# Performance work log

Hardware: AMD Instinct MI355X
Metric: run time of the kernel (lower is better)

## Reference

```python
import jax, jax.numpy as jnp
import numpy as np

DIM = 1024
NUM_HEADS = 16
HEAD_DIM = DIM // NUM_HEADS
SCALE = HEAD_DIM ** -0.5


def setup_inputs() -> dict:
    key = jax.random.key(0)
    ks = jax.random.split(key, 12)
    B, N, M, C = 4, 512, 2048, DIM
    x = jax.random.normal(ks[0], (B, N, C), dtype=jnp.float32)
    context = jax.random.normal(ks[1], (B, M, C), dtype=jnp.float32)
    mask = jax.random.randint(ks[2], (B, M), 0, 2, dtype=jnp.int32)
    mask = mask.at[:, 0].set(1)  # ensure at least one valid key per row
    w = 0.02
    Wq = jax.random.normal(ks[3], (C, C), dtype=jnp.float32) * w
    bq = jnp.zeros((C,), dtype=jnp.float32)
    Wk = jax.random.normal(ks[4], (C, C), dtype=jnp.float32) * w
    bk = jnp.zeros((C,), dtype=jnp.float32)
    Wv = jax.random.normal(ks[5], (C, C), dtype=jnp.float32) * w
    bv = jnp.zeros((C,), dtype=jnp.float32)
    Wo = jax.random.normal(ks[6], (C, C), dtype=jnp.float32) * w
    bo = jnp.zeros((C,), dtype=jnp.float32)
    return {"x": x, "context": context, "ctx_key_padding_mask": mask,
            "Wq": Wq, "bq": bq, "Wk": Wk, "bk": bk,
            "Wv": Wv, "bv": bv, "Wo": Wo, "bo": bo}


def reference(x, context, ctx_key_padding_mask, Wq, bq, Wk, bk, Wv, bv, Wo, bo):
    B, N, C = x.shape
    M = context.shape[1]
    H, D = NUM_HEADS, HEAD_DIM
    # torch nn.Linear: y = x @ W.T + b
    q = (x @ Wq.T + bq).reshape(B, N, H, D)
    k = (context @ Wk.T + bk).reshape(B, M, H, D)
    v = (context @ Wv.T + bv).reshape(B, M, H, D)
    scores = jnp.einsum('bnhd,bmhd->bhnm', q, k) * SCALE  # [B,H,N,M]
    neg = jnp.finfo(scores.dtype).min
    bias = jnp.where(ctx_key_padding_mask[:, None, None, :] != 0, 0.0, neg).astype(scores.dtype)
    attn = jax.nn.softmax(scores + bias, axis=-1)
    out = jnp.einsum('bhnm,bmhd->bnhd', attn, v).reshape(B, N, C)
    return out @ Wo.T + bo
```

## Files before the change

kernel.cpp:

```cpp
#include <hip/hip_runtime.h>
#include <hip/hip_bf16.h>
#include <stdint.h>


typedef __attribute__((ext_vector_type(4))) float f32x4;
typedef __attribute__((ext_vector_type(8))) __bf16 bf16x8;
typedef __attribute__((ext_vector_type(8))) unsigned short u16x8;

#define DEVI __device__ __forceinline__

#define QSC (0.125f * 1.44269504088896f)

DEVI f32x4 mfma16(u16x8 a, u16x8 b, f32x4 c) {
  return __builtin_amdgcn_mfma_f32_16x16x32_bf16(
      __builtin_bit_cast(bf16x8, a), __builtin_bit_cast(bf16x8, b), c, 0, 0, 0);
}

DEVI unsigned short f2bf(float f) {
  union { float f; unsigned int u; } x; x.f = f;
  unsigned int u = x.u;
  return (unsigned short)((u + 0x7fffu + ((u >> 16) & 1u)) >> 16);
}

DEVI float exp2_fast(float x) {
#if __has_builtin(__builtin_amdgcn_exp2f)
  return __builtin_amdgcn_exp2f(x);
#else
  return exp2f(x);
#endif
}

DEVI void llds16(const void* g, void* l) {
  __builtin_amdgcn_global_load_lds(
      (const __attribute__((address_space(1))) void*)g,
      (__attribute__((address_space(3))) void*)l, 16, 0, 0);
}

__global__ __launch_bounds__(256)
void mask_meta(const int* __restrict__ mask, int* __restrict__ meta,
               int* __restrict__ cnt) {
  const int b = blockIdx.x;
  const int tid = threadIdx.x;
  const int* mb = mask + b * 2048;
  int v[8], s = 0;
#pragma unroll
  for (int j = 0; j < 8; ++j) { v[j] = (mb[tid * 8 + j] != 0) ? 1 : 0; s += v[j]; }
  __shared__ int sc[2][256];
  sc[0][tid] = s;
  __syncthreads();
  int src = 0;
  for (int off = 1; off < 256; off <<= 1) {
    int x = sc[src][tid];
    if (tid >= off) x += sc[src][tid - off];
    sc[src ^ 1][tid] = x;
    src ^= 1;
    __syncthreads();
  }
  const int incl = sc[src][tid];
  const int c = sc[src][255];
  int pre = incl - s;
#pragma unroll
  for (int j = 0; j < 8; ++j) {
    const int p = tid * 8 + j;
    const unsigned dst = v[j] ? (unsigned)pre : (unsigned)(c + (p - pre));
    meta[b * 2048 + p] = (int)(dst | (v[j] ? 0x80000000u : 0u));
    pre += v[j];
  }
  if (tid == 0) cnt[b] = c;
}

__global__ __launch_bounds__(256)
void cast_fused(const float* __restrict__ x, const float* __restrict__ ctx,
                const float* __restrict__ wq, const float* __restrict__ wk,
                const float* __restrict__ wv, const float* __restrict__ wo,
                const int* __restrict__ meta, const int* __restrict__ cnt,
                unsigned short* __restrict__ xb, unsigned short* __restrict__ cb,
                unsigned short* __restrict__ wqb, unsigned short* __restrict__ wkb,
                unsigned short* __restrict__ wvb, unsigned short* __restrict__ wob) {
  int bid = blockIdx.x;
  const int tid = threadIdx.x;
  if (bid >= 512 && bid < 2560) {
    const int r0 = (bid - 512) * 4;
#pragma unroll
    for (int rr = 0; rr < 4; ++rr) {
      const int r = r0 + rr;
      const int b = r >> 11;
      const unsigned mv = (unsigned)meta[r];
      const int valid = (int)(mv >> 31);
      const int dst = (int)(mv & 0x7fffffffu);
      if (!valid && dst >= ((cnt[b] + 255) & ~255)) continue;
      unsigned short* dp = cb + ((size_t)(b * 2048 + dst)) * 1024 + tid * 4;
      if (valid) {
        const float4 v = *(const float4*)(ctx + ((size_t)r) * 1024 + tid * 4);
        ushort4 o;
        o.x = f2bf(v.x); o.y = f2bf(v.y); o.z = f2bf(v.z); o.w = f2bf(v.w);
        *(ushort4*)dp = o;
      } else {
        ushort4 z; z.x = z.y = z.z = z.w = 0;
        *(ushort4*)dp = z;
      }
    }
    return;
  }
  const float* src; unsigned short* dst; float scale = 1.f;
  if (bid < 512) { src = x; dst = xb; }
  else {
    bid -= 2560;
    const int w = bid >> 8; bid &= 255;
    src = (w == 0) ? wq : (w == 1) ? wk : (w == 2) ? wv : wo;
    dst = (w == 0) ? wqb : (w == 1) ? wkb : (w == 2) ? wvb : wob;
    if (w == 0) scale = QSC;
  }
  const int e0 = bid * 4096 + tid * 4;
#pragma unroll
  for (int it = 0; it < 4; ++it) {
    const int e = e0 + it * 1024;
    const float4 v = *(const float4*)(src + e);
    ushort4 o;
    o.x = f2bf(v.x * scale); o.y = f2bf(v.y * scale);
    o.z = f2bf(v.z * scale); o.w = f2bf(v.w * scale);
    *(ushort4*)(dst + e) = o;
  }
}

DEVI void epi_store(f32x4 (&acc)[4][4], const float* __restrict__ bias,
                    float bscale, void* __restrict__ Cout,
                    int bm, int bn, int logS, int mode,
                    unsigned short* cst, int tid, int wave, int l15, int quad) {
  const int wm = wave & 1, wn = wave >> 1;
  __syncthreads();
  for (int half = 0; half < 2; ++half) {
    if (wm == half) {
#pragma unroll
      for (int mi = 0; mi < 4; ++mi)
#pragma unroll
        for (int ni = 0; ni < 4; ++ni)
#pragma unroll
          for (int r = 0; r < 4; ++r) {
            int lrow = mi * 16 + quad * 4 + r;
            int lcol = wn * 64 + ni * 16 + l15;
            unsigned short bv = f2bf(acc[mi][ni][r] + bias[bn + lcol] * bscale);
            if (mode == 0) cst[lrow * 136 + lcol] = bv;
            else           cst[lcol * 72 + lrow] = bv;
          }
    }
    __syncthreads();
    if (mode == 0) {
      int lrow = tid >> 2, cc = (tid & 3) * 32;
      int row = bm + half * 64 + lrow;
      int S = 1 << logS;
      int b = row >> logS, sl = row & (S - 1);
#pragma unroll
      for (int j = 0; j < 4; ++j) {
        int col = bn + cc + j * 8;
        int h = col >> 6, d8 = (col & 63) >> 3;
        size_t base = (((size_t)(b * 16 + h)) << logS) * 64 +
                      (size_t)(sl >> 4) * 1024 + d8 * 128 + (sl & 15) * 8;
        *(u16x8*)&((unsigned short*)Cout)[base] =
            *(const u16x8*)&cst[lrow * 136 + cc + j * 8];
      }
    } else {
      int c = tid >> 1, rc = (tid & 1) * 32;
      int gc = bn + c, h = gc >> 6, d = gc & 63;
      int b = bm >> 11;
#pragma unroll
      for (int j = 0; j < 4; ++j) {
        int key = (bm & 2047) + half * 64 + rc + j * 8;
        size_t base = (size_t)(b * 16 + h) * 131072 +
                      (size_t)(((key >> 6) * 4 + (d >> 4)) * 8 + ((key >> 3) & 7)) * 128 +
                      (d & 15) * 8;
        *(u16x8*)&((unsigned short*)Cout)[base] =
            *(const u16x8*)&cst[c * 72 + rc + j * 8];
      }
    }
    __syncthreads();
  }
}

DEVI void kv_body(const unsigned short* __restrict__ A,
                  const unsigned short* __restrict__ WK,
                  const unsigned short* __restrict__ WV,
                  const float* __restrict__ bk, const float* __restrict__ bv,
                  unsigned short* __restrict__ kh, unsigned short* __restrict__ vt,
                  int bm, int bn, unsigned short* sh) {
  constexpr int K = 1024;
  unsigned short* As = sh;
  unsigned short* Ks = sh + 128 * 64;
  unsigned short* Vs = sh + 2 * 128 * 64;

  const int tid = threadIdx.x;
  const int wave = tid >> 6, lane = tid & 63;
  const int l15 = lane & 15, quad = lane >> 4;
  const int wm = wave & 1, wn = wave >> 1;

  f32x4 ak[4][4] = {}, av[4][4] = {};

  for (int k0 = 0; k0 < K; k0 += 64) {
    __syncthreads();
#pragma unroll
    for (int c = 0; c < 4; ++c) {
      int s = c * 256 + tid;
      int m = s >> 3;
      int k8 = (s & 7) ^ (m & 7);
      llds16(A + (size_t)(bm + m) * K + k0 + k8 * 8, &As[s * 8]);
      llds16(WK + (size_t)(bn + m) * K + k0 + k8 * 8, &Ks[s * 8]);
      llds16(WV + (size_t)(bn + m) * K + k0 + k8 * 8, &Vs[s * 8]);
    }
    __syncthreads();
#pragma unroll
    for (int ks = 0; ks < 2; ++ks) {
      const int k8 = ks * 4 + quad;
      u16x8 af[4], bf[4];
#pragma unroll
      for (int i = 0; i < 4; ++i) {
        int m = wm * 64 + i * 16 + l15;
        af[i] = *(const u16x8*)(&As[(m * 8 + (k8 ^ (m & 7))) * 8]);
      }
#pragma unroll
      for (int i = 0; i < 4; ++i) {
        int n = wn * 64 + i * 16 + l15;
        bf[i] = *(const u16x8*)(&Ks[(n * 8 + (k8 ^ (n & 7))) * 8]);
      }
#pragma unroll
      for (int mi = 0; mi < 4; ++mi)
#pragma unroll
        for (int ni = 0; ni < 4; ++ni)
          ak[mi][ni] = mfma16(af[mi], bf[ni], ak[mi][ni]);
#pragma unroll
      for (int i = 0; i < 4; ++i) {
        int n = wn * 64 + i * 16 + l15;
        bf[i] = *(const u16x8*)(&Vs[(n * 8 + (k8 ^ (n & 7))) * 8]);
      }
#pragma unroll
      for (int mi = 0; mi < 4; ++mi)
#pragma unroll
        for (int ni = 0; ni < 4; ++ni)
          av[mi][ni] = mfma16(af[mi], bf[ni], av[mi][ni]);
    }
  }

  epi_store(ak, bk, 1.f, kh, bm, bn, 11, 0, sh, tid, wave, l15, quad);
  epi_store(av, bv, 1.f, vt, bm, bn, 11, 2, sh, tid, wave, l15, quad);
}

DEVI void q_body(const unsigned short* __restrict__ A,
                 const unsigned short* __restrict__ W,
                 const float* __restrict__ bias,
                 unsigned short* __restrict__ Cout,
                 int bm, int bn, unsigned short* sh) {
  constexpr int K = 1024;
  unsigned short* As = sh;
  unsigned short* Bs = sh + 128 * 64;

  const int tid = threadIdx.x;
  const int wave = tid >> 6, lane = tid & 63;
  const int l15 = lane & 15, quad = lane >> 4;
  const int wm = wave & 1, wn = wave >> 1;

  f32x4 acc[4][4] = {};

  for (int k0 = 0; k0 < K; k0 += 64) {
    __syncthreads();
#pragma unroll
    for (int c = 0; c < 4; ++c) {
      int s = c * 256 + tid;
      int m = s >> 3;
      int k8 = (s & 7) ^ (m & 7);
      llds16(A + (size_t)(bm + m) * K + k0 + k8 * 8, &As[s * 8]);
      llds16(W + (size_t)(bn + m) * K + k0 + k8 * 8, &Bs[s * 8]);
    }
    __syncthreads();
#pragma unroll
    for (int ks = 0; ks < 2; ++ks) {
      const int k8 = ks * 4 + quad;
      u16x8 af[4], bf[4];
#pragma unroll
      for (int i = 0; i < 4; ++i) {
        int m = wm * 64 + i * 16 + l15;
        af[i] = *(const u16x8*)(&As[(m * 8 + (k8 ^ (m & 7))) * 8]);
        int n = wn * 64 + i * 16 + l15;
        bf[i] = *(const u16x8*)(&Bs[(n * 8 + (k8 ^ (n & 7))) * 8]);
      }
#pragma unroll
      for (int mi = 0; mi < 4; ++mi)
#pragma unroll
        for (int ni = 0; ni < 4; ++ni)
          acc[mi][ni] = mfma16(af[mi], bf[ni], acc[mi][ni]);
    }
  }

  epi_store(acc, bias, QSC, Cout, bm, bn, 9, 0, sh, tid, wave, l15, quad);
}

__global__ __launch_bounds__(256, 2)
void gemm_qkv(const unsigned short* __restrict__ xb,
              const unsigned short* __restrict__ cb,
              const unsigned short* __restrict__ wq,
              const unsigned short* __restrict__ wk,
              const unsigned short* __restrict__ wv,
              const float* __restrict__ bq, const float* __restrict__ bk,
              const float* __restrict__ bv,
              const int* __restrict__ cnt,
              unsigned short* __restrict__ qh, unsigned short* __restrict__ kh,
              unsigned short* __restrict__ vt) {
  __shared__ __align__(16) unsigned short sh[128 * 64 * 3];
  const int id = blockIdx.x;

  const int nb0 = ((cnt[0] + 255) & ~255) >> 7;
  const int nb1 = ((cnt[1] + 255) & ~255) >> 7;
  const int nb2 = ((cnt[2] + 255) & ~255) >> 7;
  const int nb3 = ((cnt[3] + 255) & ~255) >> 7;
  const int L = nb0 + nb1 + nb2 + nb3;
  if (id < L * 8) {
    int xl = id >> 3, y = id & 7, b = 0;
    if (xl >= nb0) { xl -= nb0; b = 1;
      if (xl >= nb1) { xl -= nb1; b = 2;
        if (xl >= nb2) { xl -= nb2; b = 3; } } }
    kv_body(cb, wk, wv, bk, bv, kh, vt, b * 2048 + xl * 128, y * 128, sh);
  } else if (id < L * 8 + 128) {
    const int q = id - L * 8;
    q_body(xb, wq, bq, qh, (q & 15) * 128, (q >> 4) * 128, sh);
  }
}

__global__ __launch_bounds__(256)
void gemm_o(const unsigned short* __restrict__ A,
            const unsigned short* __restrict__ W,
            const float* __restrict__ bo, float* __restrict__ out) {
  constexpr int K = 1024;
  __shared__ __align__(16) unsigned short As[64 * 64];
  __shared__ __align__(16) unsigned short Bs[128 * 64];

  const int tid = threadIdx.x;
  const int wave = tid >> 6, lane = tid & 63;
  const int l15 = lane & 15, quad = lane >> 4;
  const int bm = blockIdx.x * 64, bn = blockIdx.y * 128;

  f32x4 acc[4][2] = {};

  for (int k0 = 0; k0 < K; k0 += 64) {
    __syncthreads();
#pragma unroll
    for (int c = 0; c < 2; ++c) {
      int s = c * 256 + tid;
      int m = s >> 3, k8 = (s & 7) ^ (m & 7);
      llds16(A + (size_t)(bm + m) * K + k0 + k8 * 8, &As[s * 8]);
    }
#pragma unroll
    for (int c = 0; c < 4; ++c) {
      int s = c * 256 + tid;
      int m = s >> 3, k8 = (s & 7) ^ (m & 7);
      llds16(W + (size_t)(bn + m) * K + k0 + k8 * 8, &Bs[s * 8]);
    }
    __syncthreads();
#pragma unroll
    for (int ks = 0; ks < 2; ++ks) {
      const int k8 = ks * 4 + quad;
      u16x8 af[4], bf[2];
#pragma unroll
      for (int i = 0; i < 4; ++i) {
        int m = i * 16 + l15;
        af[i] = *(const u16x8*)(&As[(m * 8 + (k8 ^ (m & 7))) * 8]);
      }
#pragma unroll
      for (int i = 0; i < 2; ++i) {
        int n = wave * 32 + i * 16 + l15;
        bf[i] = *(const u16x8*)(&Bs[(n * 8 + (k8 ^ (n & 7))) * 8]);
      }
#pragma unroll
      for (int mi = 0; mi < 4; ++mi)
#pragma unroll
        for (int ni = 0; ni < 2; ++ni)
          acc[mi][ni] = mfma16(af[mi], bf[ni], acc[mi][ni]);
    }
  }

#pragma unroll
  for (int mi = 0; mi < 4; ++mi)
#pragma unroll
    for (int ni = 0; ni < 2; ++ni)
#pragma unroll
      for (int r = 0; r < 4; ++r) {
        int row = bm + mi * 16 + quad * 4 + r;
        int col = bn + wave * 32 + ni * 16 + l15;
        out[(size_t)row * 1024 + col] = acc[mi][ni][r] + bo[col];
      }
}

#define PS 72
__global__ __launch_bounds__(256, 2)
void attn_kernel(const unsigned short* __restrict__ Q,
                 const unsigned short* __restrict__ K,
                 const unsigned short* __restrict__ Vt,
                 const int* __restrict__ cnt,
                 unsigned short* __restrict__ O) {
  __shared__ __align__(16) unsigned short p_lds[4][2][16 * PS];
  __shared__ float l_lds[4][64];
  __shared__ __align__(16) float o_comb[64][68];

  const int tid = threadIdx.x;
  const int wave = tid >> 6, lane = tid & 63;
  const int l15 = lane & 15, quad = lane >> 4;
  const int bh = blockIdx.x, b = bh >> 4, h = bh & 15;
  const int q0 = blockIdx.y * 64;

  const int c = cnt[b];
  const int T = (c + 255) >> 8;

  const unsigned short* Qb = Q + (size_t)bh * 32768 + (size_t)(q0 >> 4) * 1024;
  const unsigned short* Kb = K + (size_t)bh * 131072;
  const unsigned short* Vb = Vt + (size_t)bh * 131072;

  u16x8 aq[4][2];
#pragma unroll
  for (int qg = 0; qg < 4; ++qg)
#pragma unroll
    for (int ks = 0; ks < 2; ++ks)
      aq[qg][ks] = *(const u16x8*)(Qb + ((qg * 8 + ks * 4 + quad) * 16 + l15) * 8);

  f32x4 o_acc[4][4] = {};
  float l_s[4] = {0.f, 0.f, 0.f, 0.f};

  u16x8 kf[2][4];

  auto load_k = [&](int kb) {
    const int kg0 = kb >> 4;
#pragma unroll
    for (int ns = 0; ns < 4; ++ns)
#pragma unroll
      for (int ks = 0; ks < 2; ++ks)
        kf[ks][ns] = *(const u16x8*)(Kb + (((size_t)(kg0 + ns) * 8 + ks * 4 + quad) * 16 + l15) * 8);
  };

  load_k(wave * 64);

#pragma unroll 1
  for (int t = 0; t < T; ++t) {
    const int kb = wave * 64 + t * 256;
    const int kb_next = kb + (t + 1 < T ? 256 : 0);

    u16x8 vf[2][4];
    const int kt4 = (kb >> 6) * 4;
#pragma unroll
    for (int nd = 0; nd < 4; ++nd)
#pragma unroll
      for (int ks = 0; ks < 2; ++ks)
        vf[ks][nd] = *(const u16x8*)(Vb + (((size_t)(kt4 + nd) * 8 + ks * 4 + quad) * 16 + l15) * 8);

    f32x4 bfr[4];
    if (kb + 64 <= c) {
#pragma unroll
      for (int ns = 0; ns < 4; ++ns)
        bfr[ns] = f32x4{-8.f, -8.f, -8.f, -8.f};
    } else {
#pragma unroll
      for (int ns = 0; ns < 4; ++ns)
#pragma unroll
        for (int r = 0; r < 4; ++r)
          bfr[ns][r] = (kb + ns * 16 + quad * 4 + r < c) ? -8.f : -1e30f;
    }

#pragma unroll
    for (int qg = 0; qg < 4; ++qg) {
      f32x4 sfr[4];
#pragma unroll
      for (int ns = 0; ns < 4; ++ns) {
        f32x4 sa = bfr[ns];
#pragma unroll
        for (int ks = 0; ks < 2; ++ks)
          sa = mfma16(kf[ks][ns], aq[qg][ks], sa);
        sfr[ns] = sa;
      }

      if (qg == 3) load_k(kb_next);

      float rsum = 0.f;
#pragma unroll
      for (int ns = 0; ns < 4; ++ns) {
        unsigned int pr[4];
#pragma unroll
        for (int r = 0; r < 4; ++r) {
          float p = exp2_fast(sfr[ns][r]);
          unsigned int u = __builtin_bit_cast(unsigned int, p) & 0xffff0000u;
          rsum += __builtin_bit_cast(float, u);
          pr[r] = u;
        }
        uint2 pw;
        pw.x = __builtin_amdgcn_perm(pr[1], pr[0], 0x07060302u);
        pw.y = __builtin_amdgcn_perm(pr[3], pr[2], 0x07060302u);
        *(uint2*)&p_lds[wave][qg & 1][l15 * PS + ns * 16 + quad * 4] = pw;
      }
      rsum += __shfl_xor(rsum, 16, 64);
      rsum += __shfl_xor(rsum, 32, 64);
      l_s[qg] += rsum;

#pragma unroll
      for (int ks = 0; ks < 2; ++ks) {
        u16x8 pf = *(const u16x8*)&p_lds[wave][qg & 1][l15 * PS + ks * 32 + quad * 8];
#pragma unroll
        for (int nd = 0; nd < 4; ++nd)
          o_acc[qg][nd] = mfma16(pf, vf[ks][nd], o_acc[qg][nd]);
      }
    }
  }

  if (quad == 0) {
#pragma unroll
    for (int qg = 0; qg < 4; ++qg)
      l_lds[wave][qg * 16 + l15] = l_s[qg];
  }
  __syncthreads();

  for (int w = 0; w < 4; ++w) {
    if (wave == w) {
#pragma unroll
      for (int qg = 0; qg < 4; ++qg)
#pragma unroll
        for (int r = 0; r < 4; ++r) {
          const int q = qg * 16 + quad * 4 + r;
#pragma unroll
          for (int nd = 0; nd < 4; ++nd) {
            const int d = nd * 16 + l15;
            float v = o_acc[qg][nd][r];
            if (w == 0) o_comb[q][d] = v;
            else        o_comb[q][d] += v;
          }
        }
    }
    __syncthreads();
  }

  {
    const int q = tid >> 2, dc = (tid & 3) * 16;
    const float inv = 1.f / (l_lds[0][q] + l_lds[1][q] + l_lds[2][q] + l_lds[3][q]);
    unsigned short* Ob = O + ((size_t)(b * 512 + q0 + q)) * 1024 + h * 64 + dc;
    u16x8 o1, o2;
#pragma unroll
    for (int j = 0; j < 8; ++j) o1[j] = f2bf(o_comb[q][dc + j] * inv);
#pragma unroll
    for (int j = 0; j < 8; ++j) o2[j] = f2bf(o_comb[q][dc + 8 + j] * inv);
    *(u16x8*)(Ob) = o1;
    *(u16x8*)(Ob + 8) = o2;
  }
}

extern "C" void kernel_launch(void* const* d_in, const int* in_sizes, int n_in,
                              void* d_out, int out_size, void* d_ws, size_t ws_size,
                              hipStream_t stream) {
  const float* x   = (const float*)d_in[0];
  const float* ctx = (const float*)d_in[1];
  const int* mask  = (const int*)d_in[2];
  const float* Wq  = (const float*)d_in[3];
  const float* bq  = (const float*)d_in[4];
  const float* Wk  = (const float*)d_in[5];
  const float* bk  = (const float*)d_in[6];
  const float* Wv  = (const float*)d_in[7];
  const float* bv  = (const float*)d_in[8];
  const float* Wo  = (const float*)d_in[9];
  const float* bo  = (const float*)d_in[10];

  char* ws = (char*)d_ws;
  unsigned short* xb  = (unsigned short*)(ws + ((size_t)0  << 20));
  unsigned short* cb  = (unsigned short*)(ws + ((size_t)4  << 20));
  unsigned short* wqb = (unsigned short*)(ws + ((size_t)20 << 20));
  unsigned short* wkb = (unsigned short*)(ws + ((size_t)22 << 20));
  unsigned short* wvb = (unsigned short*)(ws + ((size_t)24 << 20));
  unsigned short* wob = (unsigned short*)(ws + ((size_t)26 << 20));
  unsigned short* qh  = (unsigned short*)(ws + ((size_t)28 << 20));
  unsigned short* kh  = (unsigned short*)(ws + ((size_t)32 << 20));
  unsigned short* vt  = (unsigned short*)(ws + ((size_t)48 << 20));
  unsigned short* ah  = (unsigned short*)(ws + ((size_t)64 << 20));
  int* meta           = (int*)(ws + ((size_t)68 << 20));
  int* cntp           = meta + 8192;

  mask_meta<<<4, 256, 0, stream>>>(mask, meta, cntp);
  cast_fused<<<3584, 256, 0, stream>>>(x, ctx, Wq, Wk, Wv, Wo, meta, cntp,
                                       xb, cb, wqb, wkb, wvb, wob);
  gemm_qkv<<<640, 256, 0, stream>>>(xb, cb, wqb, wkb, wvb,
                                    bq, bk, bv, cntp, qh, kh, vt);
  attn_kernel<<<dim3(64, 8), 256, 0, stream>>>(qh, kh, vt, cntp, ah);
  gemm_o<<<dim3(32, 8), 256, 0, stream>>>(ah, wob, bo, (float*)d_out);
}
```

Before: 187.0 us.

## Fuse context gather and bf16 cast into KV GEMM, merge mask scan into cast

Drops the separate pass that compacted and cast the fp32 context into a bf16 buffer. The KV GEMM now gathers fp32 context rows through a source-index table, converts them to bf16 in registers, and writes them into LDS itself. The mask prefix-scan moves into the cast kernel's first four blocks, which removes one launch. This saves a full read and write of the context intermediate. In exchange the GEMM's A-operand path goes from async global-to-LDS copies to synchronous fp32 register loads that move twice the bytes, and each KV tile over 8 column blocks redoes the fp32 reads and conversion.

After: 194.4 us. 1.04x slower.

```diff
diff --git a/kernel.cpp b/kernel.cpp
--- a/kernel.cpp
+++ b/kernel.cpp
@@ -6,6 +6,7 @@
 typedef __attribute__((ext_vector_type(4))) float f32x4;
 typedef __attribute__((ext_vector_type(8))) __bf16 bf16x8;
 typedef __attribute__((ext_vector_type(8))) unsigned short u16x8;
+typedef __attribute__((ext_vector_type(4))) unsigned int u32x4;
 
 #define DEVI __device__ __forceinline__
 
@@ -20,6 +21,14 @@
   union { float f; unsigned int u; } x; x.f = f;
   unsigned int u = x.u;
   return (unsigned short)((u + 0x7fffu + ((u >> 16) & 1u)) >> 16);
+}
+
+DEVI unsigned int pack2(float lo, float hi) {
+  unsigned int ul = __builtin_bit_cast(unsigned int, lo);
+  unsigned int uh = __builtin_bit_cast(unsigned int, hi);
+  ul += 0x7fffu + ((ul >> 16) & 1u);
+  uh += 0x7fffu + ((uh >> 16) & 1u);
+  return __builtin_amdgcn_perm(uh, ul, 0x07060302u);
 }
 
 DEVI float exp2_fast(float x) {
@@ -37,75 +46,51 @@
 }
 
 __global__ __launch_bounds__(256)
-void mask_meta(const int* __restrict__ mask, int* __restrict__ meta,
-               int* __restrict__ cnt) {
-  const int b = blockIdx.x;
-  const int tid = threadIdx.x;
-  const int* mb = mask + b * 2048;
-  int v[8], s = 0;
-#pragma unroll
-  for (int j = 0; j < 8; ++j) { v[j] = (mb[tid * 8 + j] != 0) ? 1 : 0; s += v[j]; }
-  __shared__ int sc[2][256];
-  sc[0][tid] = s;
-  __syncthreads();
-  int src = 0;
-  for (int off = 1; off < 256; off <<= 1) {
-    int x = sc[src][tid];
-    if (tid >= off) x += sc[src][tid - off];
-    sc[src ^ 1][tid] = x;
-    src ^= 1;
-    __syncthreads();
-  }
-  const int incl = sc[src][tid];
-  const int c = sc[src][255];
-  int pre = incl - s;
-#pragma unroll
-  for (int j = 0; j < 8; ++j) {
-    const int p = tid * 8 + j;
-    const unsigned dst = v[j] ? (unsigned)pre : (unsigned)(c + (p - pre));
-    meta[b * 2048 + p] = (int)(dst | (v[j] ? 0x80000000u : 0u));
-    pre += v[j];
-  }
-  if (tid == 0) cnt[b] = c;
-}
-
-__global__ __launch_bounds__(256)
-void cast_fused(const float* __restrict__ x, const float* __restrict__ ctx,
+void cast_fused(const float* __restrict__ x,
                 const float* __restrict__ wq, const float* __restrict__ wk,
                 const float* __restrict__ wv, const float* __restrict__ wo,
-                const int* __restrict__ meta, const int* __restrict__ cnt,
-                unsigned short* __restrict__ xb, unsigned short* __restrict__ cb,
+                const int* __restrict__ mask,
+                int* __restrict__ isrc, int* __restrict__ cnt,
+                unsigned short* __restrict__ xb,
                 unsigned short* __restrict__ wqb, unsigned short* __restrict__ wkb,
                 unsigned short* __restrict__ wvb, unsigned short* __restrict__ wob) {
   int bid = blockIdx.x;
   const int tid = threadIdx.x;
-  if (bid >= 512 && bid < 2560) {
-    const int r0 = (bid - 512) * 4;
-#pragma unroll
-    for (int rr = 0; rr < 4; ++rr) {
-      const int r = r0 + rr;
-      const int b = r >> 11;
-      const unsigned mv = (unsigned)meta[r];
-      const int valid = (int)(mv >> 31);
-      const int dst = (int)(mv & 0x7fffffffu);
-      if (!valid && dst >= ((cnt[b] + 255) & ~255)) continue;
-      unsigned short* dp = cb + ((size_t)(b * 2048 + dst)) * 1024 + tid * 4;
-      if (valid) {
-        const float4 v = *(const float4*)(ctx + ((size_t)r) * 1024 + tid * 4);
-        ushort4 o;
-        o.x = f2bf(v.x); o.y = f2bf(v.y); o.z = f2bf(v.z); o.w = f2bf(v.w);
-        *(ushort4*)dp = o;
-      } else {
-        ushort4 z; z.x = z.y = z.z = z.w = 0;
-        *(ushort4*)dp = z;
-      }
-    }
+  if (bid < 4) {
+    const int b = bid;
+    const int* mb = mask + b * 2048;
+    int v[8], s = 0;
+#pragma unroll
+    for (int j = 0; j < 8; ++j) { v[j] = (mb[tid * 8 + j] != 0) ? 1 : 0; s += v[j]; }
+    __shared__ int sc[2][256];
+    sc[0][tid] = s;
+    __syncthreads();
+    int src = 0;
+    for (int off = 1; off < 256; off <<= 1) {
+      int xv = sc[src][tid];
+      if (tid >= off) xv += sc[src][tid - off];
+      sc[src ^ 1][tid] = xv;
+      src ^= 1;
+      __syncthreads();
+    }
+    const int incl = sc[src][tid];
+    const int c = sc[src][255];
+    int pre = incl - s;
+#pragma unroll
+    for (int j = 0; j < 8; ++j) {
+      const int p = tid * 8 + j;
+      const int dst = v[j] ? pre : (c + (p - pre));
+      isrc[b * 2048 + dst] = v[j] ? p : -1;
+      pre += v[j];
+    }
+    if (tid == 0) cnt[b] = c;
     return;
   }
+  bid -= 4;
   const float* src; unsigned short* dst; float scale = 1.f;
   if (bid < 512) { src = x; dst = xb; }
   else {
-    bid -= 2560;
+    bid -= 512;
     const int w = bid >> 8; bid &= 255;
     src = (w == 0) ? wq : (w == 1) ? wk : (w == 2) ? wv : wo;
     dst = (w == 0) ? wqb : (w == 1) ? wkb : (w == 2) ? wvb : wob;
@@ -177,7 +162,7 @@
   }
 }
 
-DEVI void kv_body(const unsigned short* __restrict__ A,
+DEVI void kv_body(const float* __restrict__ ctx, const int* __restrict__ isrc,
                   const unsigned short* __restrict__ WK,
                   const unsigned short* __restrict__ WV,
                   const float* __restrict__ bk, const float* __restrict__ bv,
@@ -193,6 +178,17 @@
   const int l15 = lane & 15, quad = lane >> 4;
   const int wm = wave & 1, wn = wave >> 1;
 
+  const int b2048 = bm & ~2047;
+  int srcr[4];
+  const float* asrc[4];
+#pragma unroll
+  for (int c = 0; c < 4; ++c) {
+    int s = c * 256 + tid, m = s >> 3, k8 = (s & 7) ^ (m & 7);
+    int p = isrc[bm + m];
+    srcr[c] = p;
+    asrc[c] = ctx + (size_t)(b2048 + (p < 0 ? 0 : p)) * 1024 + k8 * 8;
+  }
+
   f32x4 ak[4][4] = {}, av[4][4] = {};
 
   for (int k0 = 0; k0 < K; k0 += 64) {
@@ -202,7 +198,13 @@
       int s = c * 256 + tid;
       int m = s >> 3;
       int k8 = (s & 7) ^ (m & 7);
-      llds16(A + (size_t)(bm + m) * K + k0 + k8 * 8, &As[s * 8]);
+      const float4 a0 = *(const float4*)(asrc[c] + k0);
+      const float4 a1 = *(const float4*)(asrc[c] + k0 + 4);
+      u32x4 pw;
+      pw[0] = pack2(a0.x, a0.y); pw[1] = pack2(a0.z, a0.w);
+      pw[2] = pack2(a1.x, a1.y); pw[3] = pack2(a1.z, a1.w);
+      if (srcr[c] < 0) pw = u32x4{0u, 0u, 0u, 0u};
+      *(u32x4*)&As[s * 8] = pw;
       llds16(WK + (size_t)(bn + m) * K + k0 + k8 * 8, &Ks[s * 8]);
       llds16(WV + (size_t)(bn + m) * K + k0 + k8 * 8, &Vs[s * 8]);
     }
@@ -294,7 +296,7 @@
 
 __global__ __launch_bounds__(256, 2)
 void gemm_qkv(const unsigned short* __restrict__ xb,
-              const unsigned short* __restrict__ cb,
+              const float* __restrict__ ctx, const int* __restrict__ isrc,
               const unsigned short* __restrict__ wq,
               const unsigned short* __restrict__ wk,
               const unsigned short* __restrict__ wv,
@@ -316,7 +318,7 @@
     if (xl >= nb0) { xl -= nb0; b = 1;
       if (xl >= nb1) { xl -= nb1; b = 2;
         if (xl >= nb2) { xl -= nb2; b = 3; } } }
-    kv_body(cb, wk, wv, bk, bv, kh, vt, b * 2048 + xl * 128, y * 128, sh);
+    kv_body(ctx, isrc, wk, wv, bk, bv, kh, vt, b * 2048 + xl * 128, y * 128, sh);
   } else if (id < L * 8 + 128) {
     const int q = id - L * 8;
     q_body(xb, wq, bq, qh, (q & 15) * 128, (q >> 4) * 128, sh);
@@ -561,7 +563,6 @@
 
   char* ws = (char*)d_ws;
   unsigned short* xb  = (unsigned short*)(ws + ((size_t)0  << 20));
-  unsigned short* cb  = (unsigned short*)(ws + ((size_t)4  << 20));
   unsigned short* wqb = (unsigned short*)(ws + ((size_t)20 << 20));
   unsigned short* wkb = (unsigned short*)(ws + ((size_t)22 << 20));
   unsigned short* wvb = (unsigned short*)(ws + ((size_t)24 << 20));
@@ -570,13 +571,12 @@
   unsigned short* kh  = (unsigned short*)(ws + ((size_t)32 << 20));
   unsigned short* vt  = (unsigned short*)(ws + ((size_t)48 << 20));
   unsigned short* ah  = (unsigned short*)(ws + ((size_t)64 << 20));
-  int* meta           = (int*)(ws + ((size_t)68 << 20));
-  int* cntp           = meta + 8192;
-
-  mask_meta<<<4, 256, 0, stream>>>(mask, meta, cntp);
-  cast_fused<<<3584, 256, 0, stream>>>(x, ctx, Wq, Wk, Wv, Wo, meta, cntp,
-                                       xb, cb, wqb, wkb, wvb, wob);
-  gemm_qkv<<<640, 256, 0, stream>>>(xb, cb, wqb, wkb, wvb,
+  int* isrc           = (int*)(ws + ((size_t)68 << 20));
+  int* cntp           = isrc + 8192;
+
+  cast_fused<<<1540, 256, 0, stream>>>(x, Wq, Wk, Wv, Wo, mask, isrc, cntp,
+                                       xb, wqb, wkb, wvb, wob);
+  gemm_qkv<<<640, 256, 0, stream>>>(xb, ctx, isrc, wqb, wkb, wvb,
                                     bq, bk, bv, cntp, qh, kh, vt);
   attn_kernel<<<dim3(64, 8), 256, 0, stream>>>(qh, kh, vt, cntp, ah);
   gemm_o<<<dim3(32, 8), 256, 0, stream>>>(ah, wob, bo, (float*)d_out);
```

## Double-buffer LDS in projection GEMMs and split fused K/V blocks

Applied to the files above, without the earlier changes.

Adds a ping-pong LDS buffer to the QKV and output-projection GEMMs, so the next K-tile's global-to-LDS load is issued before the current tile's MFMAs and each iteration needs one barrier instead of two. The fused K+V block, which shared its A tile across two weight matrices, is split into separate K and V blocks that use a common generic GEMM body. The grid grows to cover the extra blocks. This gives more parallelism and latency hiding, at the cost of reading the context tile twice and using 64KB of LDS per block, which may lower occupancy.

Measured after the change: 188.8 us. No clear change (+0.9%).

```diff
diff --git a/kernel.cpp b/kernel.cpp
--- a/kernel.cpp
+++ b/kernel.cpp
@@ -177,99 +177,40 @@
   }
 }
 
-DEVI void kv_body(const unsigned short* __restrict__ A,
-                  const unsigned short* __restrict__ WK,
-                  const unsigned short* __restrict__ WV,
-                  const float* __restrict__ bk, const float* __restrict__ bv,
-                  unsigned short* __restrict__ kh, unsigned short* __restrict__ vt,
-                  int bm, int bn, unsigned short* sh) {
+DEVI void gemm_body(const unsigned short* __restrict__ A,
+                    const unsigned short* __restrict__ W,
+                    const float* __restrict__ bias, float bscale,
+                    unsigned short* __restrict__ Cout,
+                    int bm, int bn, int logS, int mode,
+                    unsigned short* sh) {
   constexpr int K = 1024;
-  unsigned short* As = sh;
-  unsigned short* Ks = sh + 128 * 64;
-  unsigned short* Vs = sh + 2 * 128 * 64;
-
   const int tid = threadIdx.x;
   const int wave = tid >> 6, lane = tid & 63;
   const int l15 = lane & 15, quad = lane >> 4;
   const int wm = wave & 1, wn = wave >> 1;
 
-  f32x4 ak[4][4] = {}, av[4][4] = {};
-
-  for (int k0 = 0; k0 < K; k0 += 64) {
-    __syncthreads();
+  auto stage = [&](int p, int k0) {
+    unsigned short* As = sh + p * 16384;
+    unsigned short* Bs = As + 8192;
 #pragma unroll
     for (int c = 0; c < 4; ++c) {
       int s = c * 256 + tid;
-      int m = s >> 3;
-      int k8 = (s & 7) ^ (m & 7);
-      llds16(A + (size_t)(bm + m) * K + k0 + k8 * 8, &As[s * 8]);
-      llds16(WK + (size_t)(bn + m) * K + k0 + k8 * 8, &Ks[s * 8]);
-      llds16(WV + (size_t)(bn + m) * K + k0 + k8 * 8, &Vs[s * 8]);
-    }
-    __syncthreads();
-#pragma unroll
-    for (int ks = 0; ks < 2; ++ks) {
-      const int k8 = ks * 4 + quad;
-      u16x8 af[4], bf[4];
-#pragma unroll
-      for (int i = 0; i < 4; ++i) {
-        int m = wm * 64 + i * 16 + l15;
-        af[i] = *(const u16x8*)(&As[(m * 8 + (k8 ^ (m & 7))) * 8]);
-      }
-#pragma unroll
-      for (int i = 0; i < 4; ++i) {
-        int n = wn * 64 + i * 16 + l15;
-        bf[i] = *(const u16x8*)(&Ks[(n * 8 + (k8 ^ (n & 7))) * 8]);
-      }
-#pragma unroll
-      for (int mi = 0; mi < 4; ++mi)
-#pragma unroll
-        for (int ni = 0; ni < 4; ++ni)
-          ak[mi][ni] = mfma16(af[mi], bf[ni], ak[mi][ni]);
-#pragma unroll
-      for (int i = 0; i < 4; ++i) {
-        int n = wn * 64 + i * 16 + l15;
-        bf[i] = *(const u16x8*)(&Vs[(n * 8 + (k8 ^ (n & 7))) * 8]);
-      }
-#pragma unroll
-      for (int mi = 0; mi < 4; ++mi)
-#pragma unroll
-        for (int ni = 0; ni < 4; ++ni)
-          av[mi][ni] = mfma16(af[mi], bf[ni], av[mi][ni]);
-    }
-  }
-
-  epi_store(ak, bk, 1.f, kh, bm, bn, 11, 0, sh, tid, wave, l15, quad);
-  epi_store(av, bv, 1.f, vt, bm, bn, 11, 2, sh, tid, wave, l15, quad);
-}
-
-DEVI void q_body(const unsigned short* __restrict__ A,
-                 const unsigned short* __restrict__ W,
-                 const float* __restrict__ bias,
-                 unsigned short* __restrict__ Cout,
-                 int bm, int bn, unsigned short* sh) {
-  constexpr int K = 1024;
-  unsigned short* As = sh;
-  unsigned short* Bs = sh + 128 * 64;
-
-  const int tid = threadIdx.x;
-  const int wave = tid >> 6, lane = tid & 63;
-  const int l15 = lane & 15, quad = lane >> 4;
-  const int wm = wave & 1, wn = wave >> 1;
-
-  f32x4 acc[4][4] = {};
-
-  for (int k0 = 0; k0 < K; k0 += 64) {
-    __syncthreads();
-#pragma unroll
-    for (int c = 0; c < 4; ++c) {
-      int s = c * 256 + tid;
-      int m = s >> 3;
-      int k8 = (s & 7) ^ (m & 7);
+      int m = s >> 3, k8 = (s & 7) ^ (m & 7);
       llds16(A + (size_t)(bm + m) * K + k0 + k8 * 8, &As[s * 8]);
       llds16(W + (size_t)(bn + m) * K + k0 + k8 * 8, &Bs[s * 8]);
     }
-    __syncthreads();
+  };
+
+  f32x4 acc[4][4] = {};
+
+  stage(0, 0);
+  __syncthreads();
+
+  int cur = 0;
+  for (int k0 = 0; k0 < K; k0 += 64) {
+    if (k0 + 64 < K) stage(cur ^ 1, k0 + 64);
+    const unsigned short* As = sh + cur * 16384;
+    const unsigned short* Bs = As + 8192;
 #pragma unroll
     for (int ks = 0; ks < 2; ++ks) {
       const int k8 = ks * 4 + quad;
@@ -287,9 +228,11 @@
         for (int ni = 0; ni < 4; ++ni)
           acc[mi][ni] = mfma16(af[mi], bf[ni], acc[mi][ni]);
     }
-  }
-
-  epi_store(acc, bias, QSC, Cout, bm, bn, 9, 0, sh, tid, wave, l15, quad);
+    __syncthreads();
+    cur ^= 1;
+  }
+
+  epi_store(acc, bias, bscale, Cout, bm, bn, logS, mode, sh, tid, wave, l15, quad);
 }
 
 __global__ __launch_bounds__(256, 2)
@@ -303,7 +246,7 @@
               const int* __restrict__ cnt,
               unsigned short* __restrict__ qh, unsigned short* __restrict__ kh,
               unsigned short* __restrict__ vt) {
-  __shared__ __align__(16) unsigned short sh[128 * 64 * 3];
+  __shared__ __align__(16) unsigned short sh[32768];
   const int id = blockIdx.x;
 
   const int nb0 = ((cnt[0] + 255) & ~255) >> 7;
@@ -311,15 +254,19 @@
   const int nb2 = ((cnt[2] + 255) & ~255) >> 7;
   const int nb3 = ((cnt[3] + 255) & ~255) >> 7;
   const int L = nb0 + nb1 + nb2 + nb3;
-  if (id < L * 8) {
-    int xl = id >> 3, y = id & 7, b = 0;
+  if (id < 2 * L * 8) {
+    const int isV = (id >= L * 8);
+    const int id2 = isV ? id - L * 8 : id;
+    int xl = id2 >> 3, y = id2 & 7, b = 0;
     if (xl >= nb0) { xl -= nb0; b = 1;
       if (xl >= nb1) { xl -= nb1; b = 2;
         if (xl >= nb2) { xl -= nb2; b = 3; } } }
-    kv_body(cb, wk, wv, bk, bv, kh, vt, b * 2048 + xl * 128, y * 128, sh);
-  } else if (id < L * 8 + 128) {
-    const int q = id - L * 8;
-    q_body(xb, wq, bq, qh, (q & 15) * 128, (q >> 4) * 128, sh);
+    const int bm = b * 2048 + xl * 128, bn = y * 128;
+    if (isV) gemm_body(cb, wv, bv, 1.f, vt, bm, bn, 11, 2, sh);
+    else     gemm_body(cb, wk, bk, 1.f, kh, bm, bn, 11, 0, sh);
+  } else if (id < 2 * L * 8 + 128) {
+    const int q = id - 2 * L * 8;
+    gemm_body(xb, wq, bq, QSC, qh, (q & 15) * 128, (q >> 4) * 128, 9, 0, sh);
   }
 }
 
@@ -328,18 +275,16 @@
             const unsigned short* __restrict__ W,
             const float* __restrict__ bo, float* __restrict__ out) {
   constexpr int K = 1024;
-  __shared__ __align__(16) unsigned short As[64 * 64];
-  __shared__ __align__(16) unsigned short Bs[128 * 64];
+  __shared__ __align__(16) unsigned short sh[24576];
 
   const int tid = threadIdx.x;
   const int wave = tid >> 6, lane = tid & 63;
   const int l15 = lane & 15, quad = lane >> 4;
   const int bm = blockIdx.x * 64, bn = blockIdx.y * 128;
 
-  f32x4 acc[4][2] = {};
-
-  for (int k0 = 0; k0 < K; k0 += 64) {
-    __syncthreads();
+  auto stage = [&](int p, int k0) {
+    unsigned short* As = sh + p * 12288;
+    unsigned short* Bs = As + 4096;
 #pragma unroll
     for (int c = 0; c < 2; ++c) {
       int s = c * 256 + tid;
@@ -352,7 +297,18 @@
       int m = s >> 3, k8 = (s & 7) ^ (m & 7);
       llds16(W + (size_t)(bn + m) * K + k0 + k8 * 8, &Bs[s * 8]);
     }
-    __syncthreads();
+  };
+
+  f32x4 acc[4][2] = {};
+
+  stage(0, 0);
+  __syncthreads();
+
+  int cur = 0;
+  for (int k0 = 0; k0 < K; k0 += 64) {
+    if (k0 + 64 < K) stage(cur ^ 1, k0 + 64);
+    const unsigned short* As = sh + cur * 12288;
+    const unsigned short* Bs = As + 4096;
 #pragma unroll
     for (int ks = 0; ks < 2; ++ks) {
       const int k8 = ks * 4 + quad;
@@ -373,6 +329,8 @@
         for (int ni = 0; ni < 2; ++ni)
           acc[mi][ni] = mfma16(af[mi], bf[ni], acc[mi][ni]);
     }
+    __syncthreads();
+    cur ^= 1;
   }
 
 #pragma unroll
@@ -576,8 +534,8 @@
   mask_meta<<<4, 256, 0, stream>>>(mask, meta, cntp);
   cast_fused<<<3584, 256, 0, stream>>>(x, ctx, Wq, Wk, Wv, Wo, meta, cntp,
                                        xb, cb, wqb, wkb, wvb, wob);
-  gemm_qkv<<<640, 256, 0, stream>>>(xb, cb, wqb, wkb, wvb,
-                                    bq, bk, bv, cntp, qh, kh, vt);
+  gemm_qkv<<<1152, 256, 0, stream>>>(xb, cb, wqb, wkb, wvb,
+                                     bq, bk, bv, cntp, qh, kh, vt);
   attn_kernel<<<dim3(64, 8), 256, 0, stream>>>(qh, kh, vt, cntp, ah);
   gemm_o<<<dim3(32, 8), 256, 0, stream>>>(ah, wob, bo, (float*)d_out);
 }
```
